# Kernel optimization log

Hardware: AMD Instinct MI355X
Metric: run time of the kernel (lower is better)

## Reference

```python
import jax, jax.numpy as jnp
import numpy as np

B, T, C = 4, 2048, 1024
H, D = 16, 64  # num_heads, head_dim; H*D == C

def setup_inputs() -> dict:
    key = jax.random.key(0)
    ks = jax.random.split(key, 5)
    s = 0.02
    return {
        "x": jax.random.normal(ks[0], (B, T, C), dtype=jnp.float32),
        "W_qkv": jax.random.normal(ks[1], (C, 3 * C), dtype=jnp.float32) * s,
        "b_qkv": jnp.zeros((3 * C,), dtype=jnp.float32),
        "W_out": jax.random.normal(ks[2], (C, C), dtype=jnp.float32) * s,
        "b_out": jnp.zeros((C,), dtype=jnp.float32),
    }

def reference(x, W_qkv, b_qkv, W_out, b_out):
    Bx, Tx, Cx = x.shape
    qkv = x @ W_qkv + b_qkv                       # [B,T,3C]
    q, k, v = jnp.split(qkv, 3, axis=-1)
    def heads(t):
        return t.reshape(Bx, Tx, H, D).transpose(0, 2, 1, 3)  # [B,H,T,D]
    q, k, v = heads(q), heads(k), heads(v)
    scale = 1.0 / jnp.sqrt(jnp.float32(D))
    attn = jnp.einsum('bhqd,bhkd->bhqk', q, k) * scale
    causal = jnp.tril(jnp.ones((Tx, Tx), dtype=bool))  # True = keep
    attn = jnp.where(causal, attn, -jnp.inf)
    attn = jax.nn.softmax(attn, axis=-1)
    out = jnp.einsum('bhqk,bhkd->bhqd', attn, v)  # [B,H,T,D]
    out = out.transpose(0, 2, 1, 3).reshape(Bx, Tx, Cx)
    return out @ W_out + b_out
```

## Files before the change

### kernel.cpp

```cpp
#include <hip/hip_runtime.h>
#include <math.h>

typedef unsigned short u16;
using bf16x8   = __attribute__((ext_vector_type(8))) __bf16;
using floatx4  = __attribute__((ext_vector_type(4))) float;
using ushortx8 = __attribute__((ext_vector_type(8))) unsigned short;
using ushortx4 = __attribute__((ext_vector_type(4))) unsigned short;
using uintx4   = __attribute__((ext_vector_type(4))) unsigned int;
using uintx2   = __attribute__((ext_vector_type(2))) unsigned int;

static __device__ __forceinline__ u16 f2bf(float f) {
  return (u16)((__float_as_uint(f) + 0x8000u) >> 16);
}
static __device__ __forceinline__ unsigned int pk2bf(float lo, float hi) {
#if __has_builtin(__builtin_amdgcn_cvt_pk_bf16_f32)
  typedef __attribute__((ext_vector_type(2))) __bf16 bf16x2_t;
  bf16x2_t r = __builtin_amdgcn_cvt_pk_bf16_f32(lo, hi);
  return *(unsigned int*)&r;
#else
  return __builtin_amdgcn_perm(__float_as_uint(hi) + 0x8000u,
                               __float_as_uint(lo) + 0x8000u, 0x07060302u);
#endif
}
static __device__ __forceinline__ float fast_exp2(float x) {
#if __has_builtin(__builtin_amdgcn_exp2f)
  return __builtin_amdgcn_exp2f(x);
#else
  return exp2f(x);
#endif
}
static __device__ __forceinline__ float fast_rcp(float x) {
#if __has_builtin(__builtin_amdgcn_rcpf)
  return __builtin_amdgcn_rcpf(x);
#else
  return 1.0f / x;
#endif
}
static __device__ __forceinline__ void gload_lds16(const void* g, void* l) {
  __builtin_amdgcn_global_load_lds(
      (const __attribute__((address_space(1))) unsigned int*)g,
      (__attribute__((address_space(3))) unsigned int*)l, 16, 0, 0);
}

__global__ __launch_bounds__(256) void cvt_bf16(const float* __restrict__ x,
                                                u16* __restrict__ y) {
  const int i = (blockIdx.x * 256 + threadIdx.x) * 8;
  floatx4 f0 = *(const floatx4*)(x + i);
  floatx4 f1 = *(const floatx4*)(x + i + 4);
  uintx4 u;
  u[0] = pk2bf(f0[0], f0[1]); u[1] = pk2bf(f0[2], f0[3]);
  u[2] = pk2bf(f1[0], f1[1]); u[3] = pk2bf(f1[2], f1[3]);
  *(uintx4*)(y + i) = u;
}

__global__ __launch_bounds__(256) void transW(const float* __restrict__ W,
                                              u16* __restrict__ WT, int K, int N) {
  __shared__ float tile[64][68];
  const int t = threadIdx.x;
  const int kb = blockIdx.y * 64, nb = blockIdx.x * 64;
  {
    const int kl = t >> 2, nc = (t & 3) * 16;
    const float* src = W + (size_t)(kb + kl) * N + nb + nc;
    #pragma unroll
    for (int c = 0; c < 4; c++)
      *(floatx4*)&tile[kl][nc + c * 4] = *(const floatx4*)(src + c * 4);
  }
  __syncthreads();
  {
    const int nl = t >> 2, kc = (t & 3) * 16;
    uintx4 u0, u1;
    #pragma unroll
    for (int j = 0; j < 4; j++)
      u0[j] = pk2bf(tile[kc + 2 * j][nl], tile[kc + 2 * j + 1][nl]);
    #pragma unroll
    for (int j = 0; j < 4; j++)
      u1[j] = pk2bf(tile[kc + 8 + 2 * j][nl], tile[kc + 9 + 2 * j][nl]);
    u16* dst = WT + (size_t)(nb + nl) * K + kb + kc;
    *(uintx4*)dst = u0;
    *(uintx4*)(dst + 8) = u1;
  }
}

template <int OUT>
__global__ __launch_bounds__(256) void gemm128(
    const u16* __restrict__ A, const u16* __restrict__ Bt,
    const float* __restrict__ bias,
    u16* __restrict__ Qb, u16* __restrict__ Kb, u16* __restrict__ Vt,
    float* __restrict__ Out, int N, int K)
{
  __shared__ u16 As[128 * 64];
  __shared__ u16 Bs[128 * 64];

  const int tid  = threadIdx.x;
  const int wave = tid >> 6, lane = tid & 63;
  const int quad = lane >> 4, l15 = lane & 15;
  const int lrow = lane >> 3;
  const int scol = ((lane & 7) ^ lrow) * 8;

  const int rowBase = blockIdx.y * 128;
  const int colBase = blockIdx.x * 128;
  const int wRow = (wave >> 1) * 64;
  const int wCol = (wave & 1) * 64;

  floatx4 acc[4][4];
  #pragma unroll
  for (int mt = 0; mt < 4; mt++)
    #pragma unroll
    for (int nt = 0; nt < 4; nt++)
      acc[mt][nt] = floatx4{0.f, 0.f, 0.f, 0.f};

  const u16* Ap = A  + (size_t)(rowBase + (wave * 4) * 8 + lrow) * K + scol;
  const u16* Bp = Bt + (size_t)(colBase + (wave * 4) * 8 + lrow) * K + scol;

  for (int k0 = 0; k0 < K; k0 += 64) {
    __syncthreads();
    #pragma unroll
    for (int i = 0; i < 4; i++) {
      const int c = wave * 4 + i;
      gload_lds16(Ap + (size_t)(i * 8) * K + k0, &As[c * 512]);
      gload_lds16(Bp + (size_t)(i * 8) * K + k0, &Bs[c * 512]);
    }
    __syncthreads();

    #pragma unroll
    for (int ks = 0; ks < 2; ks++) {
      bf16x8 a[4], b[4];
      #pragma unroll
      for (int mt = 0; mt < 4; mt++) {
        const int row = wRow + mt * 16 + l15;
        a[mt] = *(const bf16x8*)&As[row * 64 + ((((ks << 2) | quad) ^ (l15 & 7)) << 3)];
      }
      #pragma unroll
      for (int nt = 0; nt < 4; nt++) {
        const int row = wCol + nt * 16 + l15;
        b[nt] = *(const bf16x8*)&Bs[row * 64 + ((((ks << 2) | quad) ^ (l15 & 7)) << 3)];
      }
      #pragma unroll
      for (int mt = 0; mt < 4; mt++)
        #pragma unroll
        for (int nt = 0; nt < 4; nt++)
          acc[mt][nt] = __builtin_amdgcn_mfma_f32_16x16x32_bf16(a[mt], b[nt], acc[mt][nt], 0, 0, 0);
    }
  }

  if constexpr (OUT == 0) {
    const int which = colBase >> 10;
    const int cb = colBase & 1023;
    const float qscale = 0.18033688011112042f;
    #pragma unroll
    for (int mt = 0; mt < 4; mt++) {
      const int gm0 = rowBase + wRow + mt * 16 + quad * 4;
      const int bb = gm0 >> 11, t0 = gm0 & 2047;
      #pragma unroll
      for (int nt = 0; nt < 4; nt++) {
        const int gn = colBase + wCol + nt * 16 + l15;
        const int gl = cb + wCol + nt * 16 + l15;
        const float bv = bias[gn];
        const int h = gl >> 6, d = gl & 63;
        const int bh = bb * 16 + h;
        if (which == 2) {
          ushortx4 pk;
          #pragma unroll
          for (int r = 0; r < 4; r++) pk[r] = f2bf(acc[mt][nt][r] + bv);
          *(ushortx4*)&Vt[((size_t)bh * 64 + d) * 2048 + t0] = pk;
        } else if (which == 0) {
          #pragma unroll
          for (int r = 0; r < 4; r++)
            Qb[((size_t)bh * 2048 + t0 + r) * 64 + d] = f2bf((acc[mt][nt][r] + bv) * qscale);
        } else {
          #pragma unroll
          for (int r = 0; r < 4; r++)
            Kb[((size_t)bh * 2048 + t0 + r) * 64 + d] = f2bf(acc[mt][nt][r] + bv);
        }
      }
    }
  } else {
    #pragma unroll
    for (int mt = 0; mt < 4; mt++)
      #pragma unroll
      for (int nt = 0; nt < 4; nt++) {
        const int gm = rowBase + wRow + mt * 16 + quad * 4;
        const int gn = colBase + wCol + nt * 16 + l15;
        const float bv = bias[gn];
        #pragma unroll
        for (int r = 0; r < 4; r++)
          Out[(size_t)(gm + r) * N + gn] = acc[mt][nt][r] + bv;
      }
  }
}

__global__ __launch_bounds__(256) void attn_fa(
    const u16* __restrict__ Qb, const u16* __restrict__ Kb,
    const u16* __restrict__ Vt, u16* __restrict__ Ob)
{
  __shared__ u16 Qs[128 * 64];
  __shared__ u16 Ks[64 * 64], Vs[64 * 64];

  const int tid  = threadIdx.x;
  const int wave = tid >> 6, lane = tid & 63;
  const int quad = lane >> 4, l15 = lane & 15;
  const int lrow = lane >> 3;
  const int scol = ((lane & 7) ^ lrow) * 8;

  u16* Pt = &Qs[wave * 16 * 72];

  const int bh    = blockIdx.x;
  const int qt    = 15 - (int)blockIdx.y;
  const int qbase = qt * 128;

  const u16* Qp = Qb + (size_t)bh * 2048 * 64;
  const u16* Kp = Kb + (size_t)bh * 2048 * 64;
  const u16* Vp = Vt + (size_t)bh * 64 * 2048;

  #pragma unroll
  for (int i = 0; i < 4; i++) {
    const int c = wave * 4 + i;
    gload_lds16(Qp + (size_t)(qbase + c * 8 + lrow) * 64 + scol, &Qs[c * 512]);
  }
  __syncthreads();

  const int swA0 = (quad ^ (l15 & 7)) * 8;
  const int swA1 = ((4 + quad) ^ (l15 & 7)) * 8;
  bf16x8 aq[2][2];
  #pragma unroll
  for (int mt = 0; mt < 2; mt++) {
    const int row = wave * 32 + mt * 16 + l15;
    aq[mt][0] = *(const bf16x8*)&Qs[row * 64 + swA0];
    aq[mt][1] = *(const bf16x8*)&Qs[row * 64 + swA1];
  }

  floatx4 o[2][4];
  #pragma unroll
  for (int mt = 0; mt < 2; mt++)
    #pragma unroll
    for (int dt = 0; dt < 4; dt++) o[mt][dt] = floatx4{0.f, 0.f, 0.f, 0.f};
  float lsum[2] = {0.f, 0.f};

  const int rowmax = qbase + wave * 32 + 31;
  const int nk = 2 * qt + 2;
  for (int kt = 0; kt < nk; kt++) {
    const int kbase = kt * 64;
    __syncthreads();
    #pragma unroll
    for (int i = 0; i < 2; i++) {
      const int c = wave * 2 + i;
      gload_lds16(Kp + (size_t)(kbase + c * 8 + lrow) * 64 + scol, &Ks[c * 512]);
      gload_lds16(Vp + (size_t)(c * 8 + lrow) * 2048 + kbase + scol, &Vs[c * 512]);
    }
    __syncthreads();

    if (kbase > rowmax) continue;

    bf16x8 kf[4][2], vf[4][2];
    #pragma unroll
    for (int ct = 0; ct < 4; ct++) {
      const int row = ct * 16 + l15;
      kf[ct][0] = *(const bf16x8*)&Ks[row * 64 + swA0];
      kf[ct][1] = *(const bf16x8*)&Ks[row * 64 + swA1];
      vf[ct][0] = *(const bf16x8*)&Vs[row * 64 + swA0];
      vf[ct][1] = *(const bf16x8*)&Vs[row * 64 + swA1];
    }

    #pragma unroll
    for (int mt = 0; mt < 2; mt++) {
      const int rowmin = qbase + wave * 32 + mt * 16;
      if (kbase > rowmin + 15) continue;
      const bool needmask = (kbase + 63 > rowmin);

      floatx4 st[4];
      #pragma unroll
      for (int ct = 0; ct < 4; ct++) {
        floatx4 z = floatx4{0.f, 0.f, 0.f, 0.f};
        z      = __builtin_amdgcn_mfma_f32_16x16x32_bf16(kf[ct][0], aq[mt][0], z, 0, 0, 0);
        st[ct] = __builtin_amdgcn_mfma_f32_16x16x32_bf16(kf[ct][1], aq[mt][1], z, 0, 0, 0);
      }

      const int qg = rowmin + l15;
      float ls = 0.f;
      #pragma unroll
      for (int ct = 0; ct < 4; ct++) {
        float p0 = fast_exp2(st[ct][0]), p1 = fast_exp2(st[ct][1]);
        float p2 = fast_exp2(st[ct][2]), p3 = fast_exp2(st[ct][3]);
        if (needmask) {
          const int k0i = kbase + ct * 16 + quad * 4;
          if (k0i + 0 > qg) p0 = 0.f;
          if (k0i + 1 > qg) p1 = 0.f;
          if (k0i + 2 > qg) p2 = 0.f;
          if (k0i + 3 > qg) p3 = 0.f;
        }
        ls += (p0 + p1) + (p2 + p3);
        uintx2 w;
        w[0] = pk2bf(p0, p1);
        w[1] = pk2bf(p2, p3);
        *(uintx2*)&Pt[l15 * 72 + ct * 16 + quad * 4] = w;
      }
      lsum[mt] += ls;

      const bf16x8 pb0 = *(const bf16x8*)&Pt[l15 * 72 + quad * 8];
      const bf16x8 pb1 = *(const bf16x8*)&Pt[l15 * 72 + 32 + quad * 8];
      #pragma unroll
      for (int dt = 0; dt < 4; dt++) {
        o[mt][dt] = __builtin_amdgcn_mfma_f32_16x16x32_bf16(vf[dt][0], pb0, o[mt][dt], 0, 0, 0);
        o[mt][dt] = __builtin_amdgcn_mfma_f32_16x16x32_bf16(vf[dt][1], pb1, o[mt][dt], 0, 0, 0);
      }
    }
  }

  const int bb = bh >> 4, h = bh & 15;
  #pragma unroll
  for (int mt = 0; mt < 2; mt++) {
    float l = lsum[mt];
    l += __shfl_xor(l, 16);
    l += __shfl_xor(l, 32);
    const float linv = fast_rcp(l);
    const int t = qbase + wave * 32 + mt * 16 + l15;
    u16* dst = Ob + ((size_t)(bb * 2048 + t)) * 1024 + h * 64 + quad * 4;
    #pragma unroll
    for (int dt = 0; dt < 4; dt++) {
      uintx2 w;
      w[0] = pk2bf(o[mt][dt][0] * linv, o[mt][dt][1] * linv);
      w[1] = pk2bf(o[mt][dt][2] * linv, o[mt][dt][3] * linv);
      *(uintx2*)(dst + dt * 16) = w;
    }
  }
}

extern "C" void kernel_launch(void* const* d_in, const int* in_sizes, int n_in,
                              void* d_out, int out_size, void* d_ws, size_t ws_size,
                              hipStream_t stream) {
  const float* x    = (const float*)d_in[0];
  const float* Wqkv = (const float*)d_in[1];
  const float* bqkv = (const float*)d_in[2];
  const float* Wout = (const float*)d_in[3];
  const float* bout = (const float*)d_in[4];

  const size_t NB = (size_t)8192 * 1024;
  u16* Xb  = (u16*)d_ws;
  u16* WqT = Xb + NB;
  u16* Qb  = WqT + (size_t)3072 * 1024;
  u16* Kb  = Qb + NB;
  u16* Vt  = Kb + NB;

  cvt_bf16<<<4096, 256, 0, stream>>>(x, Xb);
  transW<<<dim3(48, 16), 256, 0, stream>>>(Wqkv, WqT, 1024, 3072);
  gemm128<0><<<dim3(24, 64), 256, 0, stream>>>(
      Xb, WqT, bqkv, Qb, Kb, Vt, nullptr, 3072, 1024);
  attn_fa<<<dim3(64, 16), 256, 0, stream>>>(Qb, Kb, Vt, Xb);
  transW<<<dim3(16, 16), 256, 0, stream>>>(Wout, WqT, 1024, 1024);
  gemm128<1><<<dim3(8, 64), 256, 0, stream>>>(
      Xb, WqT, bout, nullptr, nullptr, nullptr, (float*)d_out, 1024, 1024);
}
```

Measured before the change: 258.3 us.

## Fuse prep kernels, vectorize GEMM epilogues, double-buffer K/V tiles in attention

Merges the x conversion and both weight transposes into one launch, so the output-projection weight gets its own workspace buffer. In the GEMM, Q/K/out blocks swap the MFMA operand order so each lane holds 4 contiguous columns, which allows vectorized bias loads and packed stores instead of scattered scalar stores. The attention kernel double-buffers the K/V LDS tiles, prefetching the next tile while the current one is computed, which removes one barrier per iteration. The cost is more LDS in attention and duplicated GEMM main-loop code.

```diff
diff --git a/kernel.cpp b/kernel.cpp
--- a/kernel.cpp
+++ b/kernel.cpp
@@ -42,22 +42,10 @@
       (__attribute__((address_space(3))) unsigned int*)l, 16, 0, 0);
 }
 
-__global__ __launch_bounds__(256) void cvt_bf16(const float* __restrict__ x,
-                                                u16* __restrict__ y) {
-  const int i = (blockIdx.x * 256 + threadIdx.x) * 8;
-  floatx4 f0 = *(const floatx4*)(x + i);
-  floatx4 f1 = *(const floatx4*)(x + i + 4);
-  uintx4 u;
-  u[0] = pk2bf(f0[0], f0[1]); u[1] = pk2bf(f0[2], f0[3]);
-  u[2] = pk2bf(f1[0], f1[1]); u[3] = pk2bf(f1[2], f1[3]);
-  *(uintx4*)(y + i) = u;
-}
-
-__global__ __launch_bounds__(256) void transW(const float* __restrict__ W,
-                                              u16* __restrict__ WT, int K, int N) {
-  __shared__ float tile[64][68];
-  const int t = threadIdx.x;
-  const int kb = blockIdx.y * 64, nb = blockIdx.x * 64;
+static __device__ __forceinline__ void transW_tile(
+    const float* __restrict__ W, u16* __restrict__ WT, int K, int N,
+    int bx, int by, float (*tile)[68], int t) {
+  const int kb = by * 64, nb = bx * 64;
   {
     const int kl = t >> 2, nc = (t & 3) * 16;
     const float* src = W + (size_t)(kb + kl) * N + nb + nc;
@@ -78,6 +66,30 @@
     u16* dst = WT + (size_t)(nb + nl) * K + kb + kc;
     *(uintx4*)dst = u0;
     *(uintx4*)(dst + 8) = u1;
+  }
+}
+
+__global__ __launch_bounds__(256) void prep(
+    const float* __restrict__ x, const float* __restrict__ Wqkv,
+    const float* __restrict__ Wout, u16* __restrict__ Xb,
+    u16* __restrict__ WqT, u16* __restrict__ WoT) {
+  __shared__ float tile[64][68];
+  const int blk = blockIdx.x;
+  const int t = threadIdx.x;
+  if (blk < 4096) {
+    const int i = (blk * 256 + t) * 8;
+    floatx4 f0 = *(const floatx4*)(x + i);
+    floatx4 f1 = *(const floatx4*)(x + i + 4);
+    uintx4 u;
+    u[0] = pk2bf(f0[0], f0[1]); u[1] = pk2bf(f0[2], f0[3]);
+    u[2] = pk2bf(f1[0], f1[1]); u[3] = pk2bf(f1[2], f1[3]);
+    *(uintx4*)(Xb + i) = u;
+  } else if (blk < 4096 + 768) {
+    const int b2 = blk - 4096;
+    transW_tile(Wqkv, WqT, 1024, 3072, b2 % 48, b2 / 48, tile, t);
+  } else {
+    const int b3 = blk - 4096 - 768;
+    transW_tile(Wout, WoT, 1024, 1024, b3 % 16, b3 / 16, tile, t);
   }
 }
 
@@ -104,49 +116,109 @@
 
   floatx4 acc[4][4];
   #pragma unroll
-  for (int mt = 0; mt < 4; mt++)
-    #pragma unroll
-    for (int nt = 0; nt < 4; nt++)
-      acc[mt][nt] = floatx4{0.f, 0.f, 0.f, 0.f};
+  for (int i = 0; i < 4; i++)
+    #pragma unroll
+    for (int j = 0; j < 4; j++)
+      acc[i][j] = floatx4{0.f, 0.f, 0.f, 0.f};
 
   const u16* Ap = A  + (size_t)(rowBase + (wave * 4) * 8 + lrow) * K + scol;
   const u16* Bp = Bt + (size_t)(colBase + (wave * 4) * 8 + lrow) * K + scol;
 
-  for (int k0 = 0; k0 < K; k0 += 64) {
-    __syncthreads();
-    #pragma unroll
-    for (int i = 0; i < 4; i++) {
-      const int c = wave * 4 + i;
-      gload_lds16(Ap + (size_t)(i * 8) * K + k0, &As[c * 512]);
-      gload_lds16(Bp + (size_t)(i * 8) * K + k0, &Bs[c * 512]);
-    }
-    __syncthreads();
-
-    #pragma unroll
-    for (int ks = 0; ks < 2; ks++) {
-      bf16x8 a[4], b[4];
-      #pragma unroll
-      for (int mt = 0; mt < 4; mt++) {
-        const int row = wRow + mt * 16 + l15;
-        a[mt] = *(const bf16x8*)&As[row * 64 + ((((ks << 2) | quad) ^ (l15 & 7)) << 3)];
-      }
+  const bool swapped = (OUT == 1) || (colBase < 2048);
+
+  if (swapped) {
+    for (int k0 = 0; k0 < K; k0 += 64) {
+      __syncthreads();
+      #pragma unroll
+      for (int i = 0; i < 4; i++) {
+        const int c = wave * 4 + i;
+        gload_lds16(Ap + (size_t)(i * 8) * K + k0, &As[c * 512]);
+        gload_lds16(Bp + (size_t)(i * 8) * K + k0, &Bs[c * 512]);
+      }
+      __syncthreads();
+      #pragma unroll
+      for (int ks = 0; ks < 2; ks++) {
+        const int sw = (((ks << 2) | quad) ^ (l15 & 7)) << 3;
+        bf16x8 a[4], b[4];
+        #pragma unroll
+        for (int mt = 0; mt < 4; mt++)
+          a[mt] = *(const bf16x8*)&As[(wRow + mt * 16 + l15) * 64 + sw];
+        #pragma unroll
+        for (int nt = 0; nt < 4; nt++)
+          b[nt] = *(const bf16x8*)&Bs[(wCol + nt * 16 + l15) * 64 + sw];
+        #pragma unroll
+        for (int nt = 0; nt < 4; nt++)
+          #pragma unroll
+          for (int mt = 0; mt < 4; mt++)
+            acc[nt][mt] = __builtin_amdgcn_mfma_f32_16x16x32_bf16(b[nt], a[mt], acc[nt][mt], 0, 0, 0);
+      }
+    }
+    if constexpr (OUT == 0) {
+      const int which = colBase >> 10;
+      const float qscale = 0.18033688011112042f;
       #pragma unroll
       for (int nt = 0; nt < 4; nt++) {
-        const int row = wCol + nt * 16 + l15;
-        b[nt] = *(const bf16x8*)&Bs[row * 64 + ((((ks << 2) | quad) ^ (l15 & 7)) << 3)];
-      }
-      #pragma unroll
-      for (int mt = 0; mt < 4; mt++)
+        const int gn0 = colBase + wCol + nt * 16 + quad * 4;
+        const floatx4 bv = *(const floatx4*)&bias[gn0];
+        const int gl0 = (gn0 & 1023);
+        const int h = gl0 >> 6, d0 = gl0 & 63;
+        #pragma unroll
+        for (int mt = 0; mt < 4; mt++) {
+          const int gm = rowBase + wRow + mt * 16 + l15;
+          const int bb = gm >> 11, t0 = gm & 2047;
+          const int bh = bb * 16 + h;
+          uintx2 w;
+          if (which == 0) {
+            w[0] = pk2bf((acc[nt][mt][0] + bv[0]) * qscale, (acc[nt][mt][1] + bv[1]) * qscale);
+            w[1] = pk2bf((acc[nt][mt][2] + bv[2]) * qscale, (acc[nt][mt][3] + bv[3]) * qscale);
+            *(uintx2*)&Qb[((size_t)bh * 2048 + t0) * 64 + d0] = w;
+          } else {
+            w[0] = pk2bf(acc[nt][mt][0] + bv[0], acc[nt][mt][1] + bv[1]);
+            w[1] = pk2bf(acc[nt][mt][2] + bv[2], acc[nt][mt][3] + bv[3]);
+            *(uintx2*)&Kb[((size_t)bh * 2048 + t0) * 64 + d0] = w;
+          }
+        }
+      }
+    } else {
+      #pragma unroll
+      for (int nt = 0; nt < 4; nt++) {
+        const int gn0 = colBase + wCol + nt * 16 + quad * 4;
+        const floatx4 bv = *(const floatx4*)&bias[gn0];
+        #pragma unroll
+        for (int mt = 0; mt < 4; mt++) {
+          const int gm = rowBase + wRow + mt * 16 + l15;
+          floatx4 v = acc[nt][mt] + bv;
+          *(floatx4*)&Out[(size_t)gm * N + gn0] = v;
+        }
+      }
+    }
+  } else {
+    for (int k0 = 0; k0 < K; k0 += 64) {
+      __syncthreads();
+      #pragma unroll
+      for (int i = 0; i < 4; i++) {
+        const int c = wave * 4 + i;
+        gload_lds16(Ap + (size_t)(i * 8) * K + k0, &As[c * 512]);
+        gload_lds16(Bp + (size_t)(i * 8) * K + k0, &Bs[c * 512]);
+      }
+      __syncthreads();
+      #pragma unroll
+      for (int ks = 0; ks < 2; ks++) {
+        const int sw = (((ks << 2) | quad) ^ (l15 & 7)) << 3;
+        bf16x8 a[4], b[4];
+        #pragma unroll
+        for (int mt = 0; mt < 4; mt++)
+          a[mt] = *(const bf16x8*)&As[(wRow + mt * 16 + l15) * 64 + sw];
         #pragma unroll
         for (int nt = 0; nt < 4; nt++)
-          acc[mt][nt] = __builtin_amdgcn_mfma_f32_16x16x32_bf16(a[mt], b[nt], acc[mt][nt], 0, 0, 0);
-    }
-  }
-
-  if constexpr (OUT == 0) {
-    const int which = colBase >> 10;
-    const int cb = colBase & 1023;
-    const float qscale = 0.18033688011112042f;
+          b[nt] = *(const bf16x8*)&Bs[(wCol + nt * 16 + l15) * 64 + sw];
+        #pragma unroll
+        for (int mt = 0; mt < 4; mt++)
+          #pragma unroll
+          for (int nt = 0; nt < 4; nt++)
+            acc[mt][nt] = __builtin_amdgcn_mfma_f32_16x16x32_bf16(a[mt], b[nt], acc[mt][nt], 0, 0, 0);
+      }
+    }
     #pragma unroll
     for (int mt = 0; mt < 4; mt++) {
       const int gm0 = rowBase + wRow + mt * 16 + quad * 4;
@@ -154,38 +226,16 @@
       #pragma unroll
       for (int nt = 0; nt < 4; nt++) {
         const int gn = colBase + wCol + nt * 16 + l15;
-        const int gl = cb + wCol + nt * 16 + l15;
+        const int gl = gn & 1023;
         const float bv = bias[gn];
         const int h = gl >> 6, d = gl & 63;
         const int bh = bb * 16 + h;
-        if (which == 2) {
-          ushortx4 pk;
-          #pragma unroll
-          for (int r = 0; r < 4; r++) pk[r] = f2bf(acc[mt][nt][r] + bv);
-          *(ushortx4*)&Vt[((size_t)bh * 64 + d) * 2048 + t0] = pk;
-        } else if (which == 0) {
-          #pragma unroll
-          for (int r = 0; r < 4; r++)
-            Qb[((size_t)bh * 2048 + t0 + r) * 64 + d] = f2bf((acc[mt][nt][r] + bv) * qscale);
-        } else {
-          #pragma unroll
-          for (int r = 0; r < 4; r++)
-            Kb[((size_t)bh * 2048 + t0 + r) * 64 + d] = f2bf(acc[mt][nt][r] + bv);
-        }
-      }
-    }
-  } else {
-    #pragma unroll
-    for (int mt = 0; mt < 4; mt++)
-      #pragma unroll
-      for (int nt = 0; nt < 4; nt++) {
-        const int gm = rowBase + wRow + mt * 16 + quad * 4;
-        const int gn = colBase + wCol + nt * 16 + l15;
-        const float bv = bias[gn];
-        #pragma unroll
-        for (int r = 0; r < 4; r++)
-          Out[(size_t)(gm + r) * N + gn] = acc[mt][nt][r] + bv;
-      }
+        uintx2 w;
+        w[0] = pk2bf(acc[mt][nt][0] + bv, acc[mt][nt][1] + bv);
+        w[1] = pk2bf(acc[mt][nt][2] + bv, acc[mt][nt][3] + bv);
+        *(uintx2*)&Vt[((size_t)bh * 64 + d) * 2048 + t0] = w;
+      }
+    }
   }
 }
 
@@ -194,7 +244,7 @@
     const u16* __restrict__ Vt, u16* __restrict__ Ob)
 {
   __shared__ u16 Qs[128 * 64];
-  __shared__ u16 Ks[64 * 64], Vs[64 * 64];
+  __shared__ u16 Ks[2][64 * 64], Vs[2][64 * 64];
 
   const int tid  = threadIdx.x;
   const int wave = tid >> 6, lane = tid & 63;
@@ -217,6 +267,12 @@
     const int c = wave * 4 + i;
     gload_lds16(Qp + (size_t)(qbase + c * 8 + lrow) * 64 + scol, &Qs[c * 512]);
   }
+  #pragma unroll
+  for (int i = 0; i < 2; i++) {
+    const int c = wave * 2 + i;
+    gload_lds16(Kp + (size_t)(c * 8 + lrow) * 64 + scol, &Ks[0][c * 512]);
+    gload_lds16(Vp + (size_t)(c * 8 + lrow) * 2048 + scol, &Vs[0][c * 512]);
+  }
   __syncthreads();
 
   const int swA0 = (quad ^ (l15 & 7)) * 8;
@@ -228,6 +284,7 @@
     aq[mt][0] = *(const bf16x8*)&Qs[row * 64 + swA0];
     aq[mt][1] = *(const bf16x8*)&Qs[row * 64 + swA1];
   }
+  __syncthreads();
 
   floatx4 o[2][4];
   #pragma unroll
@@ -240,70 +297,74 @@
   const int nk = 2 * qt + 2;
   for (int kt = 0; kt < nk; kt++) {
     const int kbase = kt * 64;
+    const int cur = kt & 1;
+    if (kt + 1 < nk) {
+      const int nb = kbase + 64;
+      #pragma unroll
+      for (int i = 0; i < 2; i++) {
+        const int c = wave * 2 + i;
+        gload_lds16(Kp + (size_t)(nb + c * 8 + lrow) * 64 + scol, &Ks[cur ^ 1][c * 512]);
+        gload_lds16(Vp + (size_t)(c * 8 + lrow) * 2048 + nb + scol, &Vs[cur ^ 1][c * 512]);
+      }
+    }
+
+    if (kbase <= rowmax) {
+      bf16x8 kf[4][2], vf[4][2];
+      #pragma unroll
+      for (int ct = 0; ct < 4; ct++) {
+        const int row = ct * 16 + l15;
+        kf[ct][0] = *(const bf16x8*)&Ks[cur][row * 64 + swA0];
+        kf[ct][1] = *(const bf16x8*)&Ks[cur][row * 64 + swA1];
+        vf[ct][0] = *(const bf16x8*)&Vs[cur][row * 64 + swA0];
+        vf[ct][1] = *(const bf16x8*)&Vs[cur][row * 64 + swA1];
+      }
+
+      #pragma unroll
+      for (int mt = 0; mt < 2; mt++) {
+        const int rowmin = qbase + wave * 32 + mt * 16;
+        if (kbase <= rowmin + 15) {
+          const bool needmask = (kbase + 63 > rowmin);
+
+          floatx4 st[4];
+          #pragma unroll
+          for (int ct = 0; ct < 4; ct++) {
+            floatx4 z = floatx4{0.f, 0.f, 0.f, 0.f};
+            z      = __builtin_amdgcn_mfma_f32_16x16x32_bf16(kf[ct][0], aq[mt][0], z, 0, 0, 0);
+            st[ct] = __builtin_amdgcn_mfma_f32_16x16x32_bf16(kf[ct][1], aq[mt][1], z, 0, 0, 0);
+          }
+
+          const int qg = rowmin + l15;
+          float ls = 0.f;
+          #pragma unroll
+          for (int ct = 0; ct < 4; ct++) {
+            float p0 = fast_exp2(st[ct][0]), p1 = fast_exp2(st[ct][1]);
+            float p2 = fast_exp2(st[ct][2]), p3 = fast_exp2(st[ct][3]);
+            if (needmask) {
+              const int k0i = kbase + ct * 16 + quad * 4;
+              if (k0i + 0 > qg) p0 = 0.f;
+              if (k0i + 1 > qg) p1 = 0.f;
+              if (k0i + 2 > qg) p2 = 0.f;
+              if (k0i + 3 > qg) p3 = 0.f;
+            }
+            ls += (p0 + p1) + (p2 + p3);
+            uintx2 w;
+            w[0] = pk2bf(p0, p1);
+            w[1] = pk2bf(p2, p3);
+            *(uintx2*)&Pt[l15 * 72 + ct * 16 + quad * 4] = w;
+          }
+          lsum[mt] += ls;
+
+          const bf16x8 pb0 = *(const bf16x8*)&Pt[l15 * 72 + quad * 8];
+          const bf16x8 pb1 = *(const bf16x8*)&Pt[l15 * 72 + 32 + quad * 8];
+          #pragma unroll
+          for (int dt = 0; dt < 4; dt++) {
+            o[mt][dt] = __builtin_amdgcn_mfma_f32_16x16x32_bf16(vf[dt][0], pb0, o[mt][dt], 0, 0, 0);
+            o[mt][dt] = __builtin_amdgcn_mfma_f32_16x16x32_bf16(vf[dt][1], pb1, o[mt][dt], 0, 0, 0);
+          }
+        }
+      }
+    }
     __syncthreads();
-    #pragma unroll
-    for (int i = 0; i < 2; i++) {
-      const int c = wave * 2 + i;
-      gload_lds16(Kp + (size_t)(kbase + c * 8 + lrow) * 64 + scol, &Ks[c * 512]);
-      gload_lds16(Vp + (size_t)(c * 8 + lrow) * 2048 + kbase + scol, &Vs[c * 512]);
-    }
-    __syncthreads();
-
-    if (kbase > rowmax) continue;
-
-    bf16x8 kf[4][2], vf[4][2];
-    #pragma unroll
-    for (int ct = 0; ct < 4; ct++) {
-      const int row = ct * 16 + l15;
-      kf[ct][0] = *(const bf16x8*)&Ks[row * 64 + swA0];
-      kf[ct][1] = *(const bf16x8*)&Ks[row * 64 + swA1];
-      vf[ct][0] = *(const bf16x8*)&Vs[row * 64 + swA0];
-      vf[ct][1] = *(const bf16x8*)&Vs[row * 64 + swA1];
-    }
-
-    #pragma unroll
-    for (int mt = 0; mt < 2; mt++) {
-      const int rowmin = qbase + wave * 32 + mt * 16;
-      if (kbase > rowmin + 15) continue;
-      const bool needmask = (kbase + 63 > rowmin);
-
-      floatx4 st[4];
-      #pragma unroll
-      for (int ct = 0; ct < 4; ct++) {
-        floatx4 z = floatx4{0.f, 0.f, 0.f, 0.f};
-        z      = __builtin_amdgcn_mfma_f32_16x16x32_bf16(kf[ct][0], aq[mt][0], z, 0, 0, 0);
-        st[ct] = __builtin_amdgcn_mfma_f32_16x16x32_bf16(kf[ct][1], aq[mt][1], z, 0, 0, 0);
-      }
-
-      const int qg = rowmin + l15;
-      float ls = 0.f;
-      #pragma unroll
-      for (int ct = 0; ct < 4; ct++) {
-        float p0 = fast_exp2(st[ct][0]), p1 = fast_exp2(st[ct][1]);
-        float p2 = fast_exp2(st[ct][2]), p3 = fast_exp2(st[ct][3]);
-        if (needmask) {
-          const int k0i = kbase + ct * 16 + quad * 4;
-          if (k0i + 0 > qg) p0 = 0.f;
-          if (k0i + 1 > qg) p1 = 0.f;
-          if (k0i + 2 > qg) p2 = 0.f;
-          if (k0i + 3 > qg) p3 = 0.f;
-        }
-        ls += (p0 + p1) + (p2 + p3);
-        uintx2 w;
-        w[0] = pk2bf(p0, p1);
-        w[1] = pk2bf(p2, p3);
-        *(uintx2*)&Pt[l15 * 72 + ct * 16 + quad * 4] = w;
-      }
-      lsum[mt] += ls;
-
-      const bf16x8 pb0 = *(const bf16x8*)&Pt[l15 * 72 + quad * 8];
-      const bf16x8 pb1 = *(const bf16x8*)&Pt[l15 * 72 + 32 + quad * 8];
-      #pragma unroll
-      for (int dt = 0; dt < 4; dt++) {
-        o[mt][dt] = __builtin_amdgcn_mfma_f32_16x16x32_bf16(vf[dt][0], pb0, o[mt][dt], 0, 0, 0);
-        o[mt][dt] = __builtin_amdgcn_mfma_f32_16x16x32_bf16(vf[dt][1], pb1, o[mt][dt], 0, 0, 0);
-      }
-    }
   }
 
   const int bb = bh >> 4, h = bh & 15;
@@ -337,16 +398,15 @@
   const size_t NB = (size_t)8192 * 1024;
   u16* Xb  = (u16*)d_ws;
   u16* WqT = Xb + NB;
-  u16* Qb  = WqT + (size_t)3072 * 1024;
+  u16* WoT = WqT + (size_t)3072 * 1024;
+  u16* Qb  = WoT + (size_t)1024 * 1024;
   u16* Kb  = Qb + NB;
   u16* Vt  = Kb + NB;
 
-  cvt_bf16<<<4096, 256, 0, stream>>>(x, Xb);
-  transW<<<dim3(48, 16), 256, 0, stream>>>(Wqkv, WqT, 1024, 3072);
+  prep<<<5120, 256, 0, stream>>>(x, Wqkv, Wout, Xb, WqT, WoT);
   gemm128<0><<<dim3(24, 64), 256, 0, stream>>>(
       Xb, WqT, bqkv, Qb, Kb, Vt, nullptr, 3072, 1024);
   attn_fa<<<dim3(64, 16), 256, 0, stream>>>(Qb, Kb, Vt, Xb);
-  transW<<<dim3(16, 16), 256, 0, stream>>>(Wout, WqT, 1024, 1024);
   gemm128<1><<<dim3(8, 64), 256, 0, stream>>>(
-      Xb, WqT, bout, nullptr, nullptr, nullptr, (float*)d_out, 1024, 1024);
-}
+      Xb, WoT, bout, nullptr, nullptr, nullptr, (float*)d_out, 1024, 1024);
+}
```

Result: no change. 255.3 us (-1.2%).
